# Kernel optimization log

Measured on AMD Instinct MI355X. Metric: run time of the kernel, lower is better.

## Reference

```python
import jax, jax.numpy as jnp
import numpy as np

B, NQ, NK = 16, 512, 1024
CQ, CV = 128, 128
H, D = 8, 64            # nb_heads, attention_size
SCALE = float(np.sqrt(D))


def setup_inputs() -> dict:
    key = jax.random.key(0)
    ks = jax.random.split(key, 10)
    s = 0.02
    return {
        "query": jax.random.normal(ks[0], (B, NQ, CQ), jnp.float32),
        "key": jax.random.normal(ks[1], (B, NK, CV), jnp.float32),
        "c_mask": jax.random.randint(ks[2], (B, NK), 0, 2).astype(jnp.float32),
        # torch Linear params, stored as [in, out] so y = x @ W + b
        "Wq": jax.random.normal(ks[3], (CQ, H * D), jnp.float32) * s,
        "bq": jnp.zeros((H * D,), jnp.float32),
        "Wk": jax.random.normal(ks[4], (CV, H * D), jnp.float32) * s,
        "bk": jnp.zeros((H * D,), jnp.float32),
        "Wv": jax.random.normal(ks[5], (CV, H * D), jnp.float32) * s,
        "bv": jnp.zeros((H * D,), jnp.float32),
    }


def reference(query, key, c_mask, Wq, bq, Wk, bk, Wv, bv):
    # projections -> [B, N, H, D]
    q = (query @ Wq + bq).reshape(B, NQ, H, D)
    k = (key @ Wk + bk).reshape(B, NK, H, D)
    v = (key @ Wv + bv).reshape(B, NK, H, D)
    # scaled scores [B, H, NQ, NK]
    scores = jnp.einsum('bqhd,bkhd->bhqk', q / SCALE, k)
    # additive mask: c_mask [B, NK] broadcasts over heads and queries
    scores = scores - 100000.0 * (1.0 - c_mask[:, None, None, :])
    attn = jax.nn.softmax(scores, axis=-1)
    # weighted values -> [B, NQ, H, D] -> concat heads
    c = jnp.einsum('bhqk,bkhd->bqhd', attn, v)
    return c.reshape(B, NQ, H * D)
```

## Files before the change

### kernel.cpp

```cpp
#include <hip/hip_runtime.h>
#include <hip/hip_bf16.h>

#define B_  16
#define NQ_ 512
#define NK_ 1024
#define CQ_ 128
#define H_  8
#define D_  64
#define HD_ 512

typedef __attribute__((ext_vector_type(8))) short short8;
typedef __attribute__((ext_vector_type(4))) float floatx4;

__device__ __forceinline__ short f2bf(float f) {
    union { float f; unsigned u; } x; x.f = f;
    unsigned r = (x.u + 0x7fffu + ((x.u >> 16) & 1u)) >> 16;
    return (short)r;
}
__device__ __forceinline__ int f2bf_pk(float a, float b) {
    __hip_bfloat162 h = __float22bfloat162_rn(make_float2(a, b));
    int r; __builtin_memcpy(&r, &h, 4); return r;
}
__device__ __forceinline__ void async16(const short* g, short* l) {
    __builtin_amdgcn_global_load_lds(
        (const __attribute__((address_space(1))) void*)g,
        (__attribute__((address_space(3))) void*)l, 16, 0, 0);
}

__global__ void wt3_kernel(const float* __restrict__ W0, const float* __restrict__ W1,
                           const float* __restrict__ W2, short* __restrict__ T0,
                           short* __restrict__ T1, short* __restrict__ T2) {
    int gi = blockIdx.x * blockDim.x + threadIdx.x;
    int sel = gi >> 16;
    int idx = gi & 65535;
    const float* W = sel == 0 ? W0 : (sel == 1 ? W1 : W2);
    short* T = sel == 0 ? T0 : (sel == 1 ? T1 : T2);
    int n = idx >> 7, k = idx & 127;
    T[idx] = f2bf(W[k * HD_ + n]);
}

__global__ __launch_bounds__(256) void proj5_kernel(
    const float* __restrict__ query, const float* __restrict__ key_,
    const short* __restrict__ wqt, const short* __restrict__ wkt,
    const short* __restrict__ wvt,
    const float* __restrict__ bq, const float* __restrict__ bk,
    const float* __restrict__ bv,
    short* __restrict__ qs, short* __restrict__ ks, short* __restrict__ vt,
    float qscale)
{
    __shared__ __align__(16) short xsh[128 * 136];
    __shared__ __align__(16) short csh[9216];

    int bx = blockIdx.x;
    const float* X; const short* Wt; const float* bias; short* out;
    int rshift, transposed; float scale;
    if (bx < 64)       { X = query; Wt = wqt; bias = bq; out = qs; rshift = 9;  scale = qscale; transposed = 0; }
    else if (bx < 192) { bx -= 64;  X = key_; Wt = wkt; bias = bk; out = ks; rshift = 10; scale = 1.0f; transposed = 0; }
    else               { bx -= 192; X = key_; Wt = wvt; bias = bv; out = vt; rshift = 10; scale = 1.0f; transposed = 1; }

    const int tid  = threadIdx.x;
    const int w    = tid >> 6, lane = tid & 63;
    const int l15  = lane & 15, quad = lane >> 4;
    const int mbase = bx * 128;

    #pragma unroll
    for (int it = 0; it < 16; ++it) {
        const int idx = it * 256 + tid;
        const int row = idx >> 5, c4 = (idx & 31) << 2;
        float4 xv = *(const float4*)(X + (size_t)(mbase + row) * CQ_ + c4);
        *(int2*)&xsh[row * 136 + c4] = make_int2(f2bf_pk(xv.x, xv.y), f2bf_pk(xv.z, xv.w));
    }
    __syncthreads();

    short8 afr[2][4];
    #pragma unroll
    for (int mt = 0; mt < 2; ++mt) {
        const int mrow = w * 32 + mt * 16 + l15;
        #pragma unroll
        for (int kt = 0; kt < 4; ++kt)
            afr[mt][kt] = *(const short8*)&xsh[mrow * 136 + kt * 32 + quad * 8];
    }

    const int rows = 1 << rshift;
    const int b  = mbase >> rshift;
    const int r0 = mbase & (rows - 1);

    #pragma unroll
    for (int hh = 0; hh < 2; ++hh) {
        const int h = blockIdx.y * 2 + hh;
        short8 bfr[4][4];
        #pragma unroll
        for (int nt = 0; nt < 4; ++nt) {
            const short8* wrow = (const short8*)(Wt + (size_t)(h * 64 + nt * 16 + l15) * CQ_);
            #pragma unroll
            for (int kt = 0; kt < 4; ++kt) bfr[nt][kt] = wrow[kt * 4 + quad];
        }
        floatx4 acc[2][4];
        #pragma unroll
        for (int mt = 0; mt < 2; ++mt)
            #pragma unroll
            for (int nt = 0; nt < 4; ++nt) {
                floatx4 a = {0.f, 0.f, 0.f, 0.f};
                #pragma unroll
                for (int kt = 0; kt < 4; ++kt)
                    a = __builtin_amdgcn_mfma_f32_16x16x32_bf16(afr[mt][kt], bfr[nt][kt], a, 0, 0, 0);
                acc[mt][nt] = a;
            }
        __syncthreads();
        #pragma unroll
        for (int mt = 0; mt < 2; ++mt)
            #pragma unroll
            for (int nt = 0; nt < 4; ++nt) {
                const float bvv = bias[h * 64 + nt * 16 + l15];
                #pragma unroll
                for (int i = 0; i < 4; ++i) {
                    const short s = f2bf((acc[mt][nt][i] + bvv) * scale);
                    const int m = w * 32 + mt * 16 + quad * 4 + i;
                    const int n = nt * 16 + l15;
                    if (!transposed) csh[m * 72 + n]  = s;
                    else             csh[n * 136 + m] = s;
                }
            }
        __syncthreads();

        const size_t bh = (size_t)(b * H_ + h);
        if (!transposed) {
            short* dst = out + (bh * rows + r0) * D_;
            #pragma unroll
            for (int it = 0; it < 4; ++it) {
                const int idx = it * 256 + tid;
                const int row = idx >> 3, c8 = (idx & 7) * 8;
                *(short8*)(dst + idx * 8) = *(const short8*)&csh[row * 72 + c8];
            }
        } else {
            short* dst = out + bh * D_ * NK_ + r0;
            #pragma unroll
            for (int it = 0; it < 4; ++it) {
                const int idx = it * 256 + tid;
                const int row = idx >> 4, c8 = (idx & 15) * 8;
                *(short8*)(dst + (size_t)row * NK_ + c8) = *(const short8*)&csh[row * 136 + c8];
            }
        }
    }
}

__global__ __launch_bounds__(256) void attn_kernel(
    const short* __restrict__ qs, const short* __restrict__ ks,
    const short* __restrict__ vt, const float* __restrict__ cmask,
    float* __restrict__ out)
{
    __shared__ __align__(16) short kbuf[2][64 * 64];
    __shared__ __align__(16) short vbuf[2][64 * 64];
    __shared__ __align__(16) short psh[128 * 64];

    const int tid = threadIdx.x;
    const int w = tid >> 6, lane = tid & 63;
    const int l15 = lane & 15, quad = lane >> 4;

    const int bx   = blockIdx.x;
    const int xcd  = bx & 7;
    const int r_   = bx >> 3;
    const int qblk = r_ & 3;
    const int bh_i = (r_ >> 2) * 8 + xcd;
    const int h    = bh_i & 7;
    const int b    = bh_i >> 3;

    const size_t bh = (size_t)bh_i;
    const short* qb  = qs + (bh * NQ_ + (size_t)qblk * 128 + w * 32) * D_;
    const short* kb_ = ks + bh * NK_ * D_;
    const short* vb  = vt + bh * D_ * NK_;
    const float* mk  = cmask + (size_t)b * NK_;

    short8 qa[2][2];
    #pragma unroll
    for (int g = 0; g < 2; ++g) {
        const short8* qrow = (const short8*)(qb + (size_t)(g * 16 + l15) * D_);
        qa[g][0] = qrow[quad];
        qa[g][1] = qrow[4 + quad];
    }

    const int srow8 = lane >> 3, sc = lane & 7;

    float l_lane[2] = {0.f, 0.f};
    floatx4 o_acc[2][4];
    #pragma unroll
    for (int g = 0; g < 2; ++g)
        #pragma unroll
        for (int dt = 0; dt < 4; ++dt) o_acc[g][dt] = (floatx4){0.f, 0.f, 0.f, 0.f};

    #pragma unroll
    for (int j = 0; j < 2; ++j) {
        const int row = w * 16 + j * 8 + srow8;
        const int cs = sc ^ (row & 7);
        async16(kb_ + (size_t)row * D_ + cs * 8, &kbuf[0][(w * 16 + j * 8) * 64]);
        async16(vb + (size_t)row * NK_ + cs * 8, &vbuf[0][(w * 16 + j * 8) * 64]);
    }
    __syncthreads();

    for (int t = 0; t < 16; ++t) {
        const int cur = t & 1;
        if (t < 15) {
            const int nb = (t + 1) * 64, nxt = cur ^ 1;
            #pragma unroll
            for (int j = 0; j < 2; ++j) {
                const int row = w * 16 + j * 8 + srow8;
                const int cs = sc ^ (row & 7);
                async16(kb_ + (size_t)(nb + row) * D_ + cs * 8, &kbuf[nxt][(w * 16 + j * 8) * 64]);
                async16(vb + (size_t)row * NK_ + nb + cs * 8, &vbuf[nxt][(w * 16 + j * 8) * 64]);
            }
        }
        const short* kb = kbuf[cur];
        const short* vbl = vbuf[cur];
        const int kbase = t * 64;

        short8 ka[4][2];
        #pragma unroll
        for (int nt = 0; nt < 4; ++nt) {
            const int row = nt * 16 + l15;
            ka[nt][0] = *(const short8*)&kb[row * 64 + ((quad    ) ^ (row & 7)) * 8];
            ka[nt][1] = *(const short8*)&kb[row * 64 + ((4 + quad) ^ (row & 7)) * 8];
        }
        short8 vf[2][4];
        #pragma unroll
        for (int dt = 0; dt < 4; ++dt) {
            const int row = dt * 16 + l15;
            vf[0][dt] = *(const short8*)&vbl[row * 64 + ((quad    ) ^ (row & 7)) * 8];
            vf[1][dt] = *(const short8*)&vbl[row * 64 + ((4 + quad) ^ (row & 7)) * 8];
        }
        float4 m4[4];
        #pragma unroll
        for (int nt = 0; nt < 4; ++nt)
            m4[nt] = *(const float4*)(mk + kbase + nt * 16 + quad * 4);

        #pragma unroll
        for (int g = 0; g < 2; ++g) {
            floatx4 st[4];
            #pragma unroll
            for (int nt = 0; nt < 4; ++nt) {
                floatx4 a = {0.f, 0.f, 0.f, 0.f};
                a = __builtin_amdgcn_mfma_f32_16x16x32_bf16(ka[nt][1], qa[g][1], a, 0, 0, 0);
                a = __builtin_amdgcn_mfma_f32_16x16x32_bf16(ka[nt][0], qa[g][0], a, 0, 0, 0);
                st[nt] = a;
            }
            const int prow = w * 32 + g * 16 + l15;
            float psum = 0.f;
            #pragma unroll
            for (int nt = 0; nt < 4; ++nt) {
                float p0 = m4[nt].x * __builtin_amdgcn_exp2f(st[nt][0]);
                float p1 = m4[nt].y * __builtin_amdgcn_exp2f(st[nt][1]);
                float p2 = m4[nt].z * __builtin_amdgcn_exp2f(st[nt][2]);
                float p3 = m4[nt].w * __builtin_amdgcn_exp2f(st[nt][3]);
                psum += (p0 + p1) + (p2 + p3);
                int2 pk = make_int2(f2bf_pk(p0, p1), f2bf_pk(p2, p3));
                const int c16 = (2 * nt + (quad >> 1)) ^ (prow & 7);
                *(int2*)&psh[prow * 64 + c16 * 8 + (quad & 1) * 4] = pk;
            }
            l_lane[g] += psum;
        }
        #pragma unroll
        for (int g = 0; g < 2; ++g) {
            const int prow = w * 32 + g * 16 + l15;
            #pragma unroll
            for (int kt = 0; kt < 2; ++kt) {
                short8 pa = *(const short8*)&psh[prow * 64 + ((kt * 4 + quad) ^ (prow & 7)) * 8];
                #pragma unroll
                for (int dt = 0; dt < 4; ++dt)
                    o_acc[g][dt] = __builtin_amdgcn_mfma_f32_16x16x32_bf16(pa, vf[kt][dt], o_acc[g][dt], 0, 0, 0);
            }
        }
        __syncthreads();
    }

    #pragma unroll
    for (int g = 0; g < 2; ++g) {
        float ls = l_lane[g];
        ls += __shfl_xor(ls, 16);
        ls += __shfl_xor(ls, 32);
        const float linv = 1.0f / ls;
        #pragma unroll
        for (int i = 0; i < 4; ++i) {
            const float li = __shfl(linv, quad * 4 + i);
            const int qr = qblk * 128 + w * 32 + g * 16 + quad * 4 + i;
            float* orow = out + ((size_t)b * NQ_ + qr) * HD_ + h * D_;
            #pragma unroll
            for (int dt = 0; dt < 4; ++dt)
                orow[dt * 16 + l15] = o_acc[g][dt][i] * li;
        }
    }
}

extern "C" void kernel_launch(void* const* d_in, const int* in_sizes, int n_in,
                              void* d_out, int out_size, void* d_ws, size_t ws_size,
                              hipStream_t stream) {
    const float* query = (const float*)d_in[0];
    const float* key   = (const float*)d_in[1];
    const float* cmask = (const float*)d_in[2];
    const float* Wq    = (const float*)d_in[3];
    const float* bq    = (const float*)d_in[4];
    const float* Wk    = (const float*)d_in[5];
    const float* bk    = (const float*)d_in[6];
    const float* Wv    = (const float*)d_in[7];
    const float* bv    = (const float*)d_in[8];
    float* out = (float*)d_out;

    char* ws = (char*)d_ws;
    short* qs  = (short*)(ws);
    short* ks  = (short*)(ws + (size_t)( 8u << 20));
    short* vt  = (short*)(ws + (size_t)(24u << 20));
    short* wqt = (short*)(ws + (size_t)(40u << 20));
    short* wkt = (short*)(ws + (size_t)(40u << 20) + 131072 * 2);
    short* wvt = (short*)(ws + (size_t)(40u << 20) + 131072 * 4);

    wt3_kernel<<<dim3(768), dim3(256), 0, stream>>>(Wq, Wk, Wv, wqt, wkt, wvt);

    const float qscale = 0.125f * 1.44269504f;
    proj5_kernel<<<dim3(320, 4), dim3(256), 0, stream>>>(
        query, key, wqt, wkt, wvt, bq, bk, bv, qs, ks, vt, qscale);

    attn_kernel<<<dim3(512), dim3(256), 0, stream>>>(qs, ks, vt, cmask, out);
}
```

Measured before the change: 152.5 us.

## Pre-convert activations to bf16 once and vectorize attention output stores

The fp32-to-bf16 conversion of query and key moves out of the projection kernel, which ran it redundantly for each of the 4 head-pair blocks in grid y, and into the prep kernel alongside the weight transpose. The projection kernel now loads A fragments straight from global bf16 and no longer needs the LDS staging buffer or its barrier. Separately, the PV MFMA operands are swapped so each lane holds 4 contiguous output columns, which lets the epilogue write float4 stores and drop the per-row shuffles. The cost is an extra bf16 buffer write and read in global memory and a larger prep kernel.

```diff
diff --git a/kernel.cpp b/kernel.cpp
--- a/kernel.cpp
+++ b/kernel.cpp
@@ -27,20 +27,31 @@
         (__attribute__((address_space(3))) void*)l, 16, 0, 0);
 }
 
-__global__ void wt3_kernel(const float* __restrict__ W0, const float* __restrict__ W1,
-                           const float* __restrict__ W2, short* __restrict__ T0,
-                           short* __restrict__ T1, short* __restrict__ T2) {
+__global__ void prep_kernel(const float* __restrict__ W0, const float* __restrict__ W1,
+                            const float* __restrict__ W2, short* __restrict__ T0,
+                            short* __restrict__ T1, short* __restrict__ T2,
+                            const float* __restrict__ query, const float* __restrict__ key_,
+                            short* __restrict__ xq, short* __restrict__ xk) {
     int gi = blockIdx.x * blockDim.x + threadIdx.x;
-    int sel = gi >> 16;
-    int idx = gi & 65535;
-    const float* W = sel == 0 ? W0 : (sel == 1 ? W1 : W2);
-    short* T = sel == 0 ? T0 : (sel == 1 ? T1 : T2);
-    int n = idx >> 7, k = idx & 127;
-    T[idx] = f2bf(W[k * HD_ + n]);
-}
-
-__global__ __launch_bounds__(256) void proj5_kernel(
-    const float* __restrict__ query, const float* __restrict__ key_,
+    if (gi < 196608) {
+        int sel = gi >> 16;
+        int idx = gi & 65535;
+        const float* W = sel == 0 ? W0 : (sel == 1 ? W1 : W2);
+        short* T = sel == 0 ? T0 : (sel == 1 ? T1 : T2);
+        int n = idx >> 7, k = idx & 127;
+        T[idx] = f2bf(W[k * HD_ + n]);
+        return;
+    }
+    int gi2 = gi - 196608;
+    const float* src; short* dst; int idx;
+    if (gi2 < 262144) { src = query; dst = xq; idx = gi2; }
+    else              { src = key_;  dst = xk; idx = gi2 - 262144; }
+    float4 v = *(const float4*)(src + (size_t)idx * 4);
+    *(int2*)(dst + (size_t)idx * 4) = make_int2(f2bf_pk(v.x, v.y), f2bf_pk(v.z, v.w));
+}
+
+__global__ __launch_bounds__(256) void proj7_kernel(
+    const short* __restrict__ xq, const short* __restrict__ xk,
     const short* __restrict__ wqt, const short* __restrict__ wkt,
     const short* __restrict__ wvt,
     const float* __restrict__ bq, const float* __restrict__ bk,
@@ -48,37 +59,27 @@
     short* __restrict__ qs, short* __restrict__ ks, short* __restrict__ vt,
     float qscale)
 {
-    __shared__ __align__(16) short xsh[128 * 136];
     __shared__ __align__(16) short csh[9216];
 
     int bx = blockIdx.x;
-    const float* X; const short* Wt; const float* bias; short* out;
+    const short* X; const short* Wt; const float* bias; short* out;
     int rshift, transposed; float scale;
-    if (bx < 64)       { X = query; Wt = wqt; bias = bq; out = qs; rshift = 9;  scale = qscale; transposed = 0; }
-    else if (bx < 192) { bx -= 64;  X = key_; Wt = wkt; bias = bk; out = ks; rshift = 10; scale = 1.0f; transposed = 0; }
-    else               { bx -= 192; X = key_; Wt = wvt; bias = bv; out = vt; rshift = 10; scale = 1.0f; transposed = 1; }
+    if (bx < 64)       { X = xq; Wt = wqt; bias = bq; out = qs; rshift = 9;  scale = qscale; transposed = 0; }
+    else if (bx < 192) { bx -= 64;  X = xk; Wt = wkt; bias = bk; out = ks; rshift = 10; scale = 1.0f; transposed = 0; }
+    else               { bx -= 192; X = xk; Wt = wvt; bias = bv; out = vt; rshift = 10; scale = 1.0f; transposed = 1; }
 
     const int tid  = threadIdx.x;
     const int w    = tid >> 6, lane = tid & 63;
     const int l15  = lane & 15, quad = lane >> 4;
     const int mbase = bx * 128;
 
-    #pragma unroll
-    for (int it = 0; it < 16; ++it) {
-        const int idx = it * 256 + tid;
-        const int row = idx >> 5, c4 = (idx & 31) << 2;
-        float4 xv = *(const float4*)(X + (size_t)(mbase + row) * CQ_ + c4);
-        *(int2*)&xsh[row * 136 + c4] = make_int2(f2bf_pk(xv.x, xv.y), f2bf_pk(xv.z, xv.w));
-    }
-    __syncthreads();
-
     short8 afr[2][4];
     #pragma unroll
     for (int mt = 0; mt < 2; ++mt) {
-        const int mrow = w * 32 + mt * 16 + l15;
+        const short* xrow = X + (size_t)(mbase + w * 32 + mt * 16 + l15) * CQ_;
         #pragma unroll
         for (int kt = 0; kt < 4; ++kt)
-            afr[mt][kt] = *(const short8*)&xsh[mrow * 136 + kt * 32 + quad * 8];
+            afr[mt][kt] = *(const short8*)(xrow + kt * 32 + quad * 8);
     }
 
     const int rows = 1 << rshift;
@@ -265,7 +266,7 @@
                 short8 pa = *(const short8*)&psh[prow * 64 + ((kt * 4 + quad) ^ (prow & 7)) * 8];
                 #pragma unroll
                 for (int dt = 0; dt < 4; ++dt)
-                    o_acc[g][dt] = __builtin_amdgcn_mfma_f32_16x16x32_bf16(pa, vf[kt][dt], o_acc[g][dt], 0, 0, 0);
+                    o_acc[g][dt] = __builtin_amdgcn_mfma_f32_16x16x32_bf16(vf[kt][dt], pa, o_acc[g][dt], 0, 0, 0);
             }
         }
         __syncthreads();
@@ -277,14 +278,13 @@
         ls += __shfl_xor(ls, 16);
         ls += __shfl_xor(ls, 32);
         const float linv = 1.0f / ls;
-        #pragma unroll
-        for (int i = 0; i < 4; ++i) {
-            const float li = __shfl(linv, quad * 4 + i);
-            const int qr = qblk * 128 + w * 32 + g * 16 + quad * 4 + i;
-            float* orow = out + ((size_t)b * NQ_ + qr) * HD_ + h * D_;
-            #pragma unroll
-            for (int dt = 0; dt < 4; ++dt)
-                orow[dt * 16 + l15] = o_acc[g][dt][i] * li;
+        const int qr = qblk * 128 + w * 32 + g * 16 + l15;
+        float* orow = out + ((size_t)b * NQ_ + qr) * HD_ + h * D_;
+        #pragma unroll
+        for (int dt = 0; dt < 4; ++dt) {
+            float4 v = make_float4(o_acc[g][dt][0] * linv, o_acc[g][dt][1] * linv,
+                                   o_acc[g][dt][2] * linv, o_acc[g][dt][3] * linv);
+            *(float4*)(orow + dt * 16 + quad * 4) = v;
         }
     }
 }
@@ -307,15 +307,19 @@
     short* qs  = (short*)(ws);
     short* ks  = (short*)(ws + (size_t)( 8u << 20));
     short* vt  = (short*)(ws + (size_t)(24u << 20));
-    short* wqt = (short*)(ws + (size_t)(40u << 20));
-    short* wkt = (short*)(ws + (size_t)(40u << 20) + 131072 * 2);
-    short* wvt = (short*)(ws + (size_t)(40u << 20) + 131072 * 4);
-
-    wt3_kernel<<<dim3(768), dim3(256), 0, stream>>>(Wq, Wk, Wv, wqt, wkt, wvt);
+    char*  w40 = ws + (size_t)(40u << 20);
+    short* wqt = (short*)(w40);
+    short* wkt = (short*)(w40 + 131072 * 2);
+    short* wvt = (short*)(w40 + 131072 * 4);
+    short* xq  = (short*)(w40 + 131072 * 6);
+    short* xk  = (short*)(w40 + 131072 * 6 + (2u << 20));
+
+    prep_kernel<<<dim3(3840), dim3(256), 0, stream>>>(
+        Wq, Wk, Wv, wqt, wkt, wvt, query, key, xq, xk);
 
     const float qscale = 0.125f * 1.44269504f;
-    proj5_kernel<<<dim3(320, 4), dim3(256), 0, stream>>>(
-        query, key, wqt, wkt, wvt, bq, bk, bv, qs, ks, vt, qscale);
+    proj7_kernel<<<dim3(320, 4), dim3(256), 0, stream>>>(
+        xq, xk, wqt, wkt, wvt, bq, bk, bv, qs, ks, vt, qscale);
 
     attn_kernel<<<dim3(512), dim3(256), 0, stream>>>(qs, ks, vt, cmask, out);
 }
```

New measurement: 156.9 us. 1.03x slower.
